# Kernel optimization log

Measured on AMD Instinct MI355X. Metric: run time of the kernel, lower is better.

The kernel has to match this reference:

```python
import jax, jax.numpy as jnp
import numpy as np

B, D, H, E, O = 524288, 32, 64, 8, 1
H2 = H // 2


def setup_inputs() -> dict:
    key = jax.random.key(0)
    ks = jax.random.split(key, 6)
    x = jax.random.normal(ks[0], (B, D), dtype=jnp.float32)
    soft_cluster_probs = jax.random.uniform(ks[1], (B, E), dtype=jnp.float32)
    # Stacked per-expert MLP params (Dense default glorot-like scale approximated by scaled normal)
    W1 = jax.random.normal(ks[2], (E, D, H), dtype=jnp.float32) * (1.0 / np.sqrt(D))
    b1 = jnp.zeros((E, H), dtype=jnp.float32)
    W2 = jax.random.normal(ks[3], (E, H, H2), dtype=jnp.float32) * (1.0 / np.sqrt(H))
    b2 = jnp.zeros((E, H2), dtype=jnp.float32)
    W3 = jax.random.normal(ks[4], (E, H2, O), dtype=jnp.float32) * (1.0 / np.sqrt(H2))
    b3 = jnp.zeros((E, O), dtype=jnp.float32)
    return {"x": x, "soft_cluster_probs": soft_cluster_probs,
            "W1": W1, "b1": b1, "W2": W2, "b2": b2, "W3": W3, "b3": b3}


def reference(x, soft_cluster_probs, W1, b1, W2, b2, W3, b3):
    # Soft-clustering inference path: every expert processes all rows,
    # outputs combined with per-row expert weights. Dropout inactive.
    h1 = jax.nn.relu(jnp.einsum('bd,edh->ebh', x, W1) + b1[:, None, :])      # [E,B,H]
    h2 = jax.nn.relu(jnp.einsum('ebh,ehk->ebk', h1, W2) + b2[:, None, :])    # [E,B,H/2]
    eo = jax.nn.sigmoid(jnp.einsum('ebk,eko->ebo', h2, W3) + b3[:, None, :])  # [E,B,O]
    # combined = sum_e eo[e] * clustering[:, e:e+1]
    out = jnp.einsum('ebo,be->bo', eo, soft_cluster_probs)                    # [B,O]
    return out
```

## Files before the change

kernel.cpp:

```cpp
#include <hip/hip_runtime.h>


typedef __attribute__((ext_vector_type(8))) _Float16 f16x8;
typedef __attribute__((ext_vector_type(2))) __fp16 h16x2;
typedef __attribute__((ext_vector_type(4))) float f32x4;

__device__ __forceinline__ unsigned pkh(float lo, float hi) {
    union { h16x2 v; unsigned u; } t;
    t.v = __builtin_amdgcn_cvt_pkrtz(lo, hi);
    return t.u;
}

__device__ __forceinline__ unsigned relu2(unsigned a) {
    unsigned r;
    asm("v_pk_max_f16 %0, %1, 0" : "=v"(r) : "v"(a));
    return r;
}

#define MFMA32(a, b, c) __builtin_amdgcn_mfma_f32_16x16x32_f16((a), (b), (c), 0, 0, 0)

__global__ __launch_bounds__(1024, 8)
void moe_fused(const float* __restrict__ x, const float* __restrict__ probs,
               const float* __restrict__ W1, const float* __restrict__ b1,
               const float* __restrict__ W2, const float* __restrict__ b2,
               const float* __restrict__ W3, const float* __restrict__ b3,
               float* __restrict__ out) {
    __shared__ short wlds[32768];
    const int tid = threadIdx.x;
    const int w = tid >> 6, lane = tid & 63, n = lane & 15, q = lane >> 4;

    #pragma unroll
    for (int k = 0; k < 4; ++k) {
        const int F = tid + k * 1024;
        const int e = (F >> 8) & 7, s = F & 255;
        const int qq = (s >> 4) & 3, nn = s & 15;
        const float* src;
        int stride;
        if (F < 2048) {
            const int mt = s >> 6;
            const int h = 32 * (mt >> 1) + 8 * (nn >> 2) + 4 * (mt & 1) + (nn & 3);
            src = W1 + (e * 32 + 8 * qq) * 64 + h;
            stride = 64;
        } else {
            const int kb2 = (s >> 7) & 1, mt2 = (s >> 6) & 1;
            const int h2 = 8 * (nn >> 2) + 4 * mt2 + (nn & 3);
            src = W2 + (e * 64 + 32 * kb2 + 8 * qq) * 32 + h2;
            stride = 32;
        }
        union { f16x8 v; unsigned u[4]; } t;
        t.u[0] = pkh(src[0 * stride], src[1 * stride]);
        t.u[1] = pkh(src[2 * stride], src[3 * stride]);
        t.u[2] = pkh(src[4 * stride], src[5 * stride]);
        t.u[3] = pkh(src[6 * stride], src[7 * stride]);
        *(f16x8*)(wlds + F * 8) = t.v;
    }

    const int rb = blockIdx.x * 512 + w * 32;
    const float* xp0 = x + (size_t)(rb + n) * 32 + q * 8;
    const float* xp1 = xp0 + 16 * 32;
    const f32x4 xa0 = *(const f32x4*)xp0, xb0 = *(const f32x4*)(xp0 + 4);
    const f32x4 xa1 = *(const f32x4*)xp1, xb1 = *(const f32x4*)(xp1 + 4);
    union { f16x8 v; unsigned u[4]; } xf0, xf1;
    xf0.u[0] = pkh(xa0.x, xa0.y); xf0.u[1] = pkh(xa0.z, xa0.w);
    xf0.u[2] = pkh(xb0.x, xb0.y); xf0.u[3] = pkh(xb0.z, xb0.w);
    xf1.u[0] = pkh(xa1.x, xa1.y); xf1.u[1] = pkh(xa1.z, xa1.w);
    xf1.u[2] = pkh(xb1.x, xb1.y); xf1.u[3] = pkh(xb1.z, xb1.w);

    __syncthreads();

    const short* wl = wlds + (n * 8 + q * 128);
    const float* b1a = b1 + 8 * q;
    const float* b2a = b2 + 8 * q;
    const float* w3a = W3 + 8 * q;
    const float* pba = probs + (size_t)(rb + n) * 8;
    float r0 = 0.f, r1 = 0.f;

    #pragma unroll 2
    for (int e = 0; e < 8; ++e) {
        const float pb0 = pba[e], pb1 = pba[e + 128];
        const short* we = wl + e * 2048;

        union { f16x8 v; unsigned u[4]; } P0[2], P1[2];
        #pragma unroll
        for (int mt = 0; mt < 4; ++mt) {
            const f16x8 w1f = *(const f16x8*)(we + mt * 512);
            const f32x4 bf = *(const f32x4*)(b1a + e * 64 + 32 * (mt >> 1) + 4 * (mt & 1));
            const f32x4 c0 = MFMA32(w1f, xf0.v, bf);
            const f32x4 c1 = MFMA32(w1f, xf1.v, bf);
            P0[mt >> 1].u[(mt & 1) * 2 + 0] = relu2(pkh(c0.x, c0.y));
            P0[mt >> 1].u[(mt & 1) * 2 + 1] = relu2(pkh(c0.z, c0.w));
            P1[mt >> 1].u[(mt & 1) * 2 + 0] = relu2(pkh(c1.x, c1.y));
            P1[mt >> 1].u[(mt & 1) * 2 + 1] = relu2(pkh(c1.z, c1.w));
        }

        union { f16x8 v; unsigned u[4]; } PC0, PC1;
        #pragma unroll
        for (int mt2 = 0; mt2 < 2; ++mt2) {
            const f32x4 bf = *(const f32x4*)(b2a + e * 32 + 4 * mt2);
            f32x4 c0 = bf, c1 = bf;
            #pragma unroll
            for (int kb2 = 0; kb2 < 2; ++kb2) {
                const f16x8 w2f =
                    *(const f16x8*)(we + 16384 + mt2 * 512 + kb2 * 1024);
                c0 = MFMA32(w2f, P0[kb2].v, c0);
                c1 = MFMA32(w2f, P1[kb2].v, c1);
            }
            PC0.u[mt2 * 2 + 0] = relu2(pkh(c0.x, c0.y));
            PC0.u[mt2 * 2 + 1] = relu2(pkh(c0.z, c0.w));
            PC1.u[mt2 * 2 + 0] = relu2(pkh(c1.x, c1.y));
            PC1.u[mt2 * 2 + 1] = relu2(pkh(c1.z, c1.w));
        }

        const f32x4 w3lo = *(const f32x4*)(w3a + e * 32);
        const f32x4 w3hi = *(const f32x4*)(w3a + e * 32 + 4);
        union { f16x8 v; unsigned u[4]; } a3;
        a3.u[0] = pkh(w3lo.x, w3lo.y); a3.u[1] = pkh(w3lo.z, w3lo.w);
        a3.u[2] = pkh(w3hi.x, w3hi.y); a3.u[3] = pkh(w3hi.z, w3hi.w);
        const float bb = b3[e];
        const f32x4 cb = {bb, bb, bb, bb};
        const f32x4 s0 = MFMA32(a3.v, PC0.v, cb);
        const f32x4 s1 = MFMA32(a3.v, PC1.v, cb);

        r0 = fmaf(1.f / (1.f + __expf(-s0.x)), pb0, r0);
        r1 = fmaf(1.f / (1.f + __expf(-s1.x)), pb1, r1);
    }

    if (q == 0) {
        out[rb + n] = r0;
        out[rb + 16 + n] = r1;
    }
}

extern "C" void kernel_launch(void* const* d_in, const int* in_sizes, int n_in,
                              void* d_out, int out_size, void* d_ws, size_t ws_size,
                              hipStream_t stream) {
    const float* x     = (const float*)d_in[0];
    const float* probs = (const float*)d_in[1];
    const float* W1    = (const float*)d_in[2];
    const float* b1    = (const float*)d_in[3];
    const float* W2    = (const float*)d_in[4];
    const float* b2    = (const float*)d_in[5];
    const float* W3    = (const float*)d_in[6];
    const float* b3    = (const float*)d_in[7];

    const int nrows = in_sizes[0] / 32;
    hipLaunchKernelGGL(moe_fused, dim3(nrows / 512), dim3(1024), 0, stream,
                       x, probs, W1, b1, W2, b2, W3, b3, (float*)d_out);
}
```

Baseline: 155.5 us.

## Prebuild packed fp16 weight image once and bulk-copy it into LDS per block

A new single-block kernel converts W1/W2/W3 to fp16, swizzles them into the MFMA fragment layout, and packs biases into a contiguous workspace image. Each main-kernel block then copies that image into LDS with plain 16-byte loads, replacing per-block strided scalar gathers and fp32-to-fp16 conversions. Bias and W3 reads in the expert loop now come from LDS instead of global memory, and the expert loop unroll goes from 2 to 4. This adds a second kernel launch and raises LDS per block to about 68 KB, which may limit occupancy.

```diff
diff --git a/kernel.cpp b/kernel.cpp
--- a/kernel.cpp
+++ b/kernel.cpp
@@ -19,16 +19,12 @@
 
 #define MFMA32(a, b, c) __builtin_amdgcn_mfma_f32_16x16x32_f16((a), (b), (c), 0, 0, 0)
 
-__global__ __launch_bounds__(1024, 8)
-void moe_fused(const float* __restrict__ x, const float* __restrict__ probs,
-               const float* __restrict__ W1, const float* __restrict__ b1,
-               const float* __restrict__ W2, const float* __restrict__ b2,
-               const float* __restrict__ W3, const float* __restrict__ b3,
-               float* __restrict__ out) {
-    __shared__ short wlds[32768];
+__global__ __launch_bounds__(1024)
+void build_image(const float* __restrict__ W1, const float* __restrict__ b1,
+                 const float* __restrict__ W2, const float* __restrict__ b2,
+                 const float* __restrict__ W3, const float* __restrict__ b3,
+                 char* __restrict__ ws) {
     const int tid = threadIdx.x;
-    const int w = tid >> 6, lane = tid & 63, n = lane & 15, q = lane >> 4;
-
     #pragma unroll
     for (int k = 0; k < 4; ++k) {
         const int F = tid + k * 1024;
@@ -52,7 +48,45 @@
         t.u[1] = pkh(src[2 * stride], src[3 * stride]);
         t.u[2] = pkh(src[4 * stride], src[5 * stride]);
         t.u[3] = pkh(src[6 * stride], src[7 * stride]);
-        *(f16x8*)(wlds + F * 8) = t.v;
+        *(f16x8*)(ws + F * 16) = t.v;
+    }
+    if (tid < 128) {
+        const int e = tid >> 4, mt = (tid >> 2) & 3, q = tid & 3;
+        *(f32x4*)(ws + 65536 + tid * 16) =
+            *(const f32x4*)(b1 + e * 64 + 32 * (mt >> 1) + 4 * (mt & 1) + 8 * q);
+    } else if (tid < 192) {
+        const int i = tid - 128, e = i >> 3, mt2 = (i >> 2) & 1, q = i & 3;
+        *(f32x4*)(ws + 67584 + i * 16) =
+            *(const f32x4*)(b2 + e * 32 + 4 * mt2 + 8 * q);
+    } else if (tid < 224) {
+        const int i = tid - 192, e = i >> 2, q = i & 3;
+        const f32x4 lo = *(const f32x4*)(W3 + e * 32 + 8 * q);
+        const f32x4 hi = *(const f32x4*)(W3 + e * 32 + 8 * q + 4);
+        union { f16x8 v; unsigned u[4]; } a;
+        a.u[0] = pkh(lo.x, lo.y); a.u[1] = pkh(lo.z, lo.w);
+        a.u[2] = pkh(hi.x, hi.y); a.u[3] = pkh(hi.z, hi.w);
+        *(f16x8*)(ws + 68608 + i * 16) = a.v;
+    } else if (tid < 232) {
+        const int i = tid - 224;
+        *(float*)(ws + 69120 + i * 4) = b3[i];
+    }
+}
+
+__global__ __launch_bounds__(1024, 8)
+void moe_fused(const float* __restrict__ x, const float* __restrict__ probs,
+               const char* __restrict__ img, float* __restrict__ out) {
+    __shared__ __attribute__((aligned(16))) char ldsraw[69632];
+    const int tid = threadIdx.x;
+    const int w = tid >> 6, lane = tid & 63, n = lane & 15, q = lane >> 4;
+
+    #pragma unroll
+    for (int k = 0; k < 4; ++k) {
+        const int off = tid * 16 + k * 16384;
+        *(f32x4*)(ldsraw + off) = *(const f32x4*)(img + off);
+    }
+    if (tid < 226) {
+        const int off = 65536 + tid * 16;
+        *(f32x4*)(ldsraw + off) = *(const f32x4*)(img + off);
     }
 
     const int rb = blockIdx.x * 512 + w * 32;
@@ -68,14 +102,14 @@
 
     __syncthreads();
 
-    const short* wl = wlds + (n * 8 + q * 128);
-    const float* b1a = b1 + 8 * q;
-    const float* b2a = b2 + 8 * q;
-    const float* w3a = W3 + 8 * q;
+    const short* wl = (const short*)ldsraw + (n * 8 + q * 128);
+    const char* bb1 = ldsraw + 65536 + q * 16;
+    const char* bb2 = ldsraw + 67584 + q * 16;
+    const char* ba3 = ldsraw + 68608 + q * 16;
     const float* pba = probs + (size_t)(rb + n) * 8;
     float r0 = 0.f, r1 = 0.f;
 
-    #pragma unroll 2
+    #pragma unroll 4
     for (int e = 0; e < 8; ++e) {
         const float pb0 = pba[e], pb1 = pba[e + 128];
         const short* we = wl + e * 2048;
@@ -84,7 +118,7 @@
         #pragma unroll
         for (int mt = 0; mt < 4; ++mt) {
             const f16x8 w1f = *(const f16x8*)(we + mt * 512);
-            const f32x4 bf = *(const f32x4*)(b1a + e * 64 + 32 * (mt >> 1) + 4 * (mt & 1));
+            const f32x4 bf = *(const f32x4*)(bb1 + e * 256 + mt * 64);
             const f32x4 c0 = MFMA32(w1f, xf0.v, bf);
             const f32x4 c1 = MFMA32(w1f, xf1.v, bf);
             P0[mt >> 1].u[(mt & 1) * 2 + 0] = relu2(pkh(c0.x, c0.y));
@@ -96,7 +130,7 @@
         union { f16x8 v; unsigned u[4]; } PC0, PC1;
         #pragma unroll
         for (int mt2 = 0; mt2 < 2; ++mt2) {
-            const f32x4 bf = *(const f32x4*)(b2a + e * 32 + 4 * mt2);
+            const f32x4 bf = *(const f32x4*)(bb2 + e * 128 + mt2 * 64);
             f32x4 c0 = bf, c1 = bf;
             #pragma unroll
             for (int kb2 = 0; kb2 < 2; ++kb2) {
@@ -111,15 +145,11 @@
             PC1.u[mt2 * 2 + 1] = relu2(pkh(c1.z, c1.w));
         }
 
-        const f32x4 w3lo = *(const f32x4*)(w3a + e * 32);
-        const f32x4 w3hi = *(const f32x4*)(w3a + e * 32 + 4);
-        union { f16x8 v; unsigned u[4]; } a3;
-        a3.u[0] = pkh(w3lo.x, w3lo.y); a3.u[1] = pkh(w3lo.z, w3lo.w);
-        a3.u[2] = pkh(w3hi.x, w3hi.y); a3.u[3] = pkh(w3hi.z, w3hi.w);
-        const float bb = b3[e];
+        const f16x8 a3v = *(const f16x8*)(ba3 + e * 64);
+        const float bb = *(const float*)(ldsraw + 69120 + e * 4);
         const f32x4 cb = {bb, bb, bb, bb};
-        const f32x4 s0 = MFMA32(a3.v, PC0.v, cb);
-        const f32x4 s1 = MFMA32(a3.v, PC1.v, cb);
+        const f32x4 s0 = MFMA32(a3v, PC0.v, cb);
+        const f32x4 s1 = MFMA32(a3v, PC1.v, cb);
 
         r0 = fmaf(1.f / (1.f + __expf(-s0.x)), pb0, r0);
         r1 = fmaf(1.f / (1.f + __expf(-s1.x)), pb1, r1);
@@ -143,7 +173,9 @@
     const float* W3    = (const float*)d_in[6];
     const float* b3    = (const float*)d_in[7];
 
+    hipLaunchKernelGGL(build_image, dim3(1), dim3(1024), 0, stream,
+                       W1, b1, W2, b2, W3, b3, (char*)d_ws);
     const int nrows = in_sizes[0] / 32;
     hipLaunchKernelGGL(moe_fused, dim3(nrows / 512), dim3(1024), 0, stream,
-                       x, probs, W1, b1, W2, b2, W3, b3, (float*)d_out);
+                       x, probs, (const char*)d_ws, (float*)d_out);
 }
```

New measurement: 145.1 us. 6.7% less time.
